# Performance work log

Hardware: AMD Instinct MI355X
Metric: run time of the kernel (lower is better)

Reference implementation:

```python
import jax, jax.numpy as jnp
import numpy as np

EMBED_DIM = 512
N_HEADS = 8
D_K = EMBED_DIM // N_HEADS

def _xavier(key, shape):
    fan_in, fan_out = shape[1], shape[0]
    limit = np.sqrt(6.0 / (fan_in + fan_out))
    return jax.random.uniform(key, shape, jnp.float32, -limit, limit)

def setup_inputs() -> dict:
    key = jax.random.key(0)
    ks = jax.random.split(key, 8)
    B, S, D = 2, 4096, EMBED_DIM
    return {
        "q": jax.random.normal(ks[0], (B, S, D), jnp.float32),
        "k": jax.random.normal(ks[1], (B, S, D), jnp.float32),
        "v": jax.random.normal(ks[2], (B, S, D), jnp.float32),
        "W_q": _xavier(ks[3], (D, D)),
        "W_k": _xavier(ks[4], (D, D)),
        "W_v": _xavier(ks[5], (D, D)),
        "W_o": _xavier(ks[6], (D, D)),
        "b_o": jnp.zeros((D,), jnp.float32),
    }

def reference(q, k, v, W_q, W_k, W_v, W_o, b_o):
    B, Sq, D = q.shape
    Sk = k.shape[1]
    # linear projections (torch Linear: x @ W.T)
    qh = (q @ W_q.T).reshape(B, Sq, N_HEADS, D_K).transpose(0, 2, 1, 3)
    kh = (k @ W_k.T).reshape(B, Sk, N_HEADS, D_K).transpose(0, 2, 1, 3)
    vh = (v @ W_v.T).reshape(B, Sk, N_HEADS, D_K).transpose(0, 2, 1, 3)
    scores = jnp.einsum('bhqd,bhkd->bhqk', qh, kh)  # [B,H,Sq,Sk]
    causal = jnp.triu(jnp.ones((Sq, Sk), bool), k=1)
    scores = jnp.where(causal, -jnp.inf, scores)
    attn = jax.nn.softmax(scores / np.sqrt(D_K), axis=-1)
    ctx = jnp.einsum('bhqk,bhkd->bhqd', attn, vh)
    ctx = ctx.transpose(0, 2, 1, 3).reshape(B, Sq, D)
    return ctx @ W_o.T + b_o
```

## Files before the change

kernel.cpp:

```cpp
#include <hip/hip_runtime.h>

typedef _Float16 f16;
typedef _Float16 f16x8 __attribute__((ext_vector_type(8)));
typedef _Float16 f16x4 __attribute__((ext_vector_type(4)));
typedef float f32x4 __attribute__((ext_vector_type(4)));
typedef float f32x16 __attribute__((ext_vector_type(16)));

#define S_TOK 4096
#define NB 2
#define NH 8
#define DKH 64
#define DMODEL 512

static __device__ __forceinline__ f32x4 mfma16(f16x8 a, f16x8 b, f32x4 c) {
    return __builtin_amdgcn_mfma_f32_16x16x32_f16(a, b, c, 0, 0, 0);
}
static __device__ __forceinline__ f32x16 mfma32(f16x8 a, f16x8 b, f32x16 c) {
    return __builtin_amdgcn_mfma_f32_32x32x16_f16(a, b, c, 0, 0, 0);
}

__global__ __launch_bounds__(256)
void proj_fused_kernel(const float* __restrict__ qx, const float* __restrict__ kx,
                       const float* __restrict__ vx,
                       const float* __restrict__ Wqp, const float* __restrict__ Wkp,
                       const float* __restrict__ Wvp,
                       f16* __restrict__ qo, f16* __restrict__ ko, f16* __restrict__ vo)
{
    const int mode = blockIdx.z;
    const float* x = (mode == 0) ? qx : (mode == 1) ? kx : vx;
    const float* W = (mode == 0) ? Wqp : (mode == 1) ? Wkp : Wvp;
    f16* out = (mode == 0) ? qo : (mode == 1) ? ko : vo;

    __shared__ f16 As[128 * 40];
    __shared__ f16 Bs[128 * 40];
    const int m0 = blockIdx.x * 128;
    const int n0 = blockIdx.y * 128;
    const int tid = threadIdx.x;
    const int wv = tid >> 6;
    const int lane = tid & 63;
    const int lr = lane & 15, lg = lane >> 4;
    const int wm = (wv >> 1) * 64, wn = (wv & 1) * 64;

    f32x4 acc[4][4];
#pragma unroll
    for (int i = 0; i < 4; ++i)
#pragma unroll
        for (int j = 0; j < 4; ++j) acc[i][j] = f32x4{0.f, 0.f, 0.f, 0.f};

    for (int kb = 0; kb < DMODEL; kb += 32) {
#pragma unroll
        for (int c = 0; c < 2; ++c) {
            const int chunk = tid + c * 256;
            const int row = chunk >> 2;
            const int col = (chunk & 3) * 8;
            const float* ga = x + (size_t)(m0 + row) * DMODEL + kb + col;
            float4 a0 = *(const float4*)ga;
            float4 a1 = *(const float4*)(ga + 4);
            f16x8 ha = { (f16)a0.x, (f16)a0.y, (f16)a0.z, (f16)a0.w,
                         (f16)a1.x, (f16)a1.y, (f16)a1.z, (f16)a1.w };
            *(f16x8*)(As + row * 40 + col) = ha;
            const float* gb = W + (size_t)(n0 + row) * DMODEL + kb + col;
            float4 b0 = *(const float4*)gb;
            float4 b1 = *(const float4*)(gb + 4);
            f16x8 hb = { (f16)b0.x, (f16)b0.y, (f16)b0.z, (f16)b0.w,
                         (f16)b1.x, (f16)b1.y, (f16)b1.z, (f16)b1.w };
            *(f16x8*)(Bs + row * 40 + col) = hb;
        }
        __syncthreads();
        f16x8 af[4], bf[4];
#pragma unroll
        for (int i = 0; i < 4; ++i)
            af[i] = *(const f16x8*)(As + (wm + 16 * i + lr) * 40 + 8 * lg);
#pragma unroll
        for (int j = 0; j < 4; ++j)
            bf[j] = *(const f16x8*)(Bs + (wn + 16 * j + lr) * 40 + 8 * lg);
#pragma unroll
        for (int i = 0; i < 4; ++i)
#pragma unroll
            for (int j = 0; j < 4; ++j)
                acc[i][j] = mfma16(af[i], bf[j], acc[i][j]);
        __syncthreads();
    }

#pragma unroll
    for (int i = 0; i < 4; ++i) {
        const int mbase = m0 + wm + 16 * i + 4 * lg;
#pragma unroll
        for (int j = 0; j < 4; ++j) {
            const int n = n0 + wn + 16 * j + lr;
            const int h = n >> 6, dk = n & 63;
            if (mode == 2) {
                const int b = mbase >> 12;
                const int s = mbase & 4095;
                f16x4 v4;
#pragma unroll
                for (int r = 0; r < 4; ++r) v4[r] = (f16)acc[i][j][r];
                *(f16x4*)(out + ((size_t)(b * NH + h) * DKH + dk) * S_TOK + s) = v4;
            } else {
                const float sc = (mode == 0) ? 0.1803368801111244f : 1.0f;
#pragma unroll
                for (int r = 0; r < 4; ++r) {
                    const int m = mbase + r;
                    const int b = m >> 12, s = m & 4095;
                    out[((size_t)(b * NH + h) * S_TOK + s) * DKH + dk] = (f16)(acc[i][j][r] * sc);
                }
            }
        }
    }
}

__global__ __launch_bounds__(256, 3)
void attn_kernel(const f16* __restrict__ qh, const f16* __restrict__ kh,
                 const f16* __restrict__ vt, f16* __restrict__ pO, float* __restrict__ pL)
{
    __shared__ f16 Ks[2][64 * 64];
    __shared__ f16 Vs[2][64 * 64];
    __shared__ f16 Ps[4][32 * 72];

    const int bid = blockIdx.x;
    const int bh = 2 * (bid & 7) + ((bid >> 3) & 1);
    const int j = bid >> 4;
    const int tid = threadIdx.x, wv = tid >> 6, lane = tid & 63;
    const int l31 = lane & 31, h = lane >> 5;

    const f16* Qp = qh + (size_t)bh * S_TOK * DKH;
    const f16* Kp = kh + (size_t)bh * S_TOK * DKH;
    const f16* Vp = vt + (size_t)bh * DKH * S_TOK;

    const int srow = tid >> 2;
    const int s0 = (tid & 3) + 4 * ((tid >> 2) & 1);
    const int s1 = s0 ^ 4;
    const int g0 = s0 ^ (srow & 7), g1 = s1 ^ (srow & 7);
    const int ldA = srow * 64 + s0 * 8, ldB = srow * 64 + s1 * 8;
    f16* Pw = &Ps[wv][0];

    for (int seg = 0; seg < 2; ++seg) {
        const int qt = seg ? (31 - j) : j;
        const int t0 = seg ? (qt + 1) : 0;
        const int t1 = seg ? (2 * qt + 2) : (j + 1);
        const int q0 = qt * 128;
        const int qw = q0 + 32 * wv + l31;
        const int unit = (bh * 32 + qt) * 2 + seg;

        f16x8 aq[4];
#pragma unroll
        for (int s = 0; s < 4; ++s)
            aq[s] = *(const f16x8*)(Qp + (size_t)qw * DKH + 16 * s + 8 * h);

        f32x16 accO0 = {}, accO1 = {};
        float mrow = -1e20f, lrow = 0.f;

        f16x8 ka = *(const f16x8*)(Kp + (size_t)(64 * t0 + srow) * DKH + g0 * 8);
        f16x8 kb = *(const f16x8*)(Kp + (size_t)(64 * t0 + srow) * DKH + g1 * 8);
        f16x8 va = *(const f16x8*)(Vp + (size_t)srow * S_TOK + 64 * t0 + g0 * 8);
        f16x8 vb = *(const f16x8*)(Vp + (size_t)srow * S_TOK + 64 * t0 + g1 * 8);
        __syncthreads();
        *(f16x8*)(&Ks[0][ldA]) = ka;  *(f16x8*)(&Ks[0][ldB]) = kb;
        *(f16x8*)(&Vs[0][ldA]) = va;  *(f16x8*)(&Vs[0][ldB]) = vb;

        int cur = 0;
        for (int t = t0; t < t1; ++t) {
            const bool pre = (t + 1 < t1);
            f16x8 kna, knb, vna, vnb;
            if (pre) {
                kna = *(const f16x8*)(Kp + (size_t)(64 * (t + 1) + srow) * DKH + g0 * 8);
                knb = *(const f16x8*)(Kp + (size_t)(64 * (t + 1) + srow) * DKH + g1 * 8);
                vna = *(const f16x8*)(Vp + (size_t)srow * S_TOK + 64 * (t + 1) + g0 * 8);
                vnb = *(const f16x8*)(Vp + (size_t)srow * S_TOK + 64 * (t + 1) + g1 * 8);
            }
            __syncthreads();
            const f16* Kb = &Ks[cur][0];
            const f16* Vb = &Vs[cur][0];

            f32x16 accS0 = {}, accS1 = {};
            __builtin_amdgcn_s_setprio(1);
#pragma unroll
            for (int s = 0; s < 4; ++s) {
                f16x8 ak0 = *(const f16x8*)(Kb + (l31) * 64 + ((2 * s + h) ^ (l31 & 7)) * 8);
                f16x8 ak1 = *(const f16x8*)(Kb + (32 + l31) * 64 + ((2 * s + h) ^ (l31 & 7)) * 8);
                accS0 = mfma32(ak0, aq[s], accS0);
                accS1 = mfma32(ak1, aq[s], accS1);
            }
            __builtin_amdgcn_s_setprio(0);

            if (t >= 2 * qt) {
#pragma unroll
                for (int e = 0; e < 16; ++e) {
                    const int kvb = 64 * t + (e & 3) + 8 * (e >> 2) + 4 * h;
                    accS0[e] = (kvb > qw) ? -1e30f : accS0[e];
                    accS1[e] = (kvb + 32 > qw) ? -1e30f : accS1[e];
                }
            }

            float tm = -1e30f;
#pragma unroll
            for (int e = 0; e < 16; ++e) tm = fmaxf(tm, fmaxf(accS0[e], accS1[e]));
            tm = fmaxf(tm, __shfl_xor(tm, 32));
            if (!__all(tm <= mrow + 8.f)) {
                const float mn = fmaxf(mrow, tm);
                const float sf = exp2f(mrow - mn);
                lrow *= sf;
                accO0 *= sf;  accO1 *= sf;
                mrow = mn;
            }
            float ts = 0.f;
#pragma unroll
            for (int g = 0; g < 4; ++g) {
                f16x4 u, u2;
#pragma unroll
                for (int r = 0; r < 4; ++r) {
                    const float p = exp2f(accS0[4 * g + r] - mrow);
                    ts += p;
                    u[r] = (f16)p;
                    const float pq = exp2f(accS1[4 * g + r] - mrow);
                    ts += pq;
                    u2[r] = (f16)pq;
                }
                *(f16x4*)(Pw + l31 * 72 + 8 * g + 4 * h) = u;
                *(f16x4*)(Pw + l31 * 72 + 32 + 8 * g + 4 * h) = u2;
            }
            ts += __shfl_xor(ts, 32);
            lrow += ts;

            __builtin_amdgcn_s_setprio(1);
#pragma unroll
            for (int s = 0; s < 4; ++s) {
                f16x8 bp = *(const f16x8*)(Pw + l31 * 72 + 16 * s + 8 * h);
                f16x8 av0 = *(const f16x8*)(Vb + (l31) * 64 + ((2 * s + h) ^ (l31 & 7)) * 8);
                f16x8 av1 = *(const f16x8*)(Vb + (32 + l31) * 64 + ((2 * s + h) ^ (l31 & 7)) * 8);
                accO0 = mfma32(av0, bp, accO0);
                accO1 = mfma32(av1, bp, accO1);
            }
            __builtin_amdgcn_s_setprio(0);

            if (pre) {
                *(f16x8*)(&Ks[cur ^ 1][ldA]) = kna;  *(f16x8*)(&Ks[cur ^ 1][ldB]) = knb;
                *(f16x8*)(&Vs[cur ^ 1][ldA]) = vna;  *(f16x8*)(&Vs[cur ^ 1][ldB]) = vnb;
            }
            cur ^= 1;
        }

        const float invl = (lrow > 0.f) ? (1.f / lrow) : 0.f;
        f16* Ob = pO + ((size_t)unit * 128 + (32 * wv + l31)) * DKH;
#pragma unroll
        for (int g = 0; g < 4; ++g) {
            f16x4 o0, o1;
#pragma unroll
            for (int r = 0; r < 4; ++r) {
                o0[r] = (f16)(accO0[4 * g + r] * invl);
                o1[r] = (f16)(accO1[4 * g + r] * invl);
            }
            *(f16x4*)(Ob + 8 * g + 4 * h) = o0;
            *(f16x4*)(Ob + 32 + 8 * g + 4 * h) = o1;
        }
        if (h == 0)
            pL[unit * 128 + 32 * wv + l31] =
                (lrow > 0.f) ? (mrow + __log2f(lrow)) : -1e30f;
    }
}

__global__ __launch_bounds__(256)
void merge_kernel(const f16* __restrict__ pO, const float* __restrict__ pL,
                  f16* __restrict__ ctx)
{
    const int tid = threadIdx.x;
    const int R = blockIdx.x * 32 + (tid >> 3);
    const int dkg = tid & 7;
    const int bh = R >> 12, q = R & 4095;
    const int qt = q >> 7, qi = q & 127;
    const int u0 = (bh * 32 + qt) * 2, u1 = u0 + 1;

    const float L0 = pL[u0 * 128 + qi];
    const float L1 = pL[u1 * 128 + qi];
    const float Lm = fmaxf(L0, L1);
    const float w0 = exp2f(L0 - Lm);
    const float w1 = exp2f(L1 - Lm);
    const float inv = 1.f / (w0 + w1);

    f16x8 a = *(const f16x8*)(pO + ((size_t)u0 * 128 + qi) * DKH + dkg * 8);
    f16x8 b = *(const f16x8*)(pO + ((size_t)u1 * 128 + qi) * DKH + dkg * 8);
    f16x8 o;
#pragma unroll
    for (int i = 0; i < 8; ++i)
        o[i] = (f16)((w0 * (float)a[i] + w1 * (float)b[i]) * inv);

    const int bb = bh >> 3, hh = bh & 7;
    *(f16x8*)(ctx + ((size_t)(bb * S_TOK + q)) * DMODEL + hh * DKH + dkg * 8) = o;
}

__global__ __launch_bounds__(256)
void oproj_kernel(const f16* __restrict__ A, const float* __restrict__ W,
                  const float* __restrict__ bias, float* __restrict__ out)
{
    __shared__ f16 As[128 * 40];
    __shared__ f16 Bs[128 * 40];
    const int m0 = blockIdx.x * 128;
    const int n0 = blockIdx.y * 128;
    const int tid = threadIdx.x;
    const int wv = tid >> 6;
    const int lane = tid & 63;
    const int lr = lane & 15, lg = lane >> 4;
    const int wm = (wv >> 1) * 64, wn = (wv & 1) * 64;

    f32x4 acc[4][4];
#pragma unroll
    for (int i = 0; i < 4; ++i)
#pragma unroll
        for (int j = 0; j < 4; ++j) acc[i][j] = f32x4{0.f, 0.f, 0.f, 0.f};

    for (int kb = 0; kb < DMODEL; kb += 32) {
#pragma unroll
        for (int c = 0; c < 2; ++c) {
            const int chunk = tid + c * 256;
            const int row = chunk >> 2;
            const int col = (chunk & 3) * 8;
            *(f16x8*)(As + row * 40 + col) =
                *(const f16x8*)(A + (size_t)(m0 + row) * DMODEL + kb + col);
            const float* gb = W + (size_t)(n0 + row) * DMODEL + kb + col;
            float4 b0 = *(const float4*)gb;
            float4 b1 = *(const float4*)(gb + 4);
            f16x8 hb = { (f16)b0.x, (f16)b0.y, (f16)b0.z, (f16)b0.w,
                         (f16)b1.x, (f16)b1.y, (f16)b1.z, (f16)b1.w };
            *(f16x8*)(Bs + row * 40 + col) = hb;
        }
        __syncthreads();
        f16x8 af[4], bf[4];
#pragma unroll
        for (int i = 0; i < 4; ++i)
            af[i] = *(const f16x8*)(As + (wm + 16 * i + lr) * 40 + 8 * lg);
#pragma unroll
        for (int j = 0; j < 4; ++j)
            bf[j] = *(const f16x8*)(Bs + (wn + 16 * j + lr) * 40 + 8 * lg);
#pragma unroll
        for (int i = 0; i < 4; ++i)
#pragma unroll
            for (int j = 0; j < 4; ++j)
                acc[i][j] = mfma16(af[i], bf[j], acc[i][j]);
        __syncthreads();
    }

#pragma unroll
    for (int i = 0; i < 4; ++i) {
        const int mbase = m0 + wm + 16 * i + 4 * lg;
#pragma unroll
        for (int j = 0; j < 4; ++j) {
            const int n = n0 + wn + 16 * j + lr;
            const float bn = bias[n];
#pragma unroll
            for (int r = 0; r < 4; ++r) {
                const int m = mbase + r;
                out[(size_t)m * DMODEL + n] = acc[i][j][r] + bn;
            }
        }
    }
}

extern "C" void kernel_launch(void* const* d_in, const int* in_sizes, int n_in,
                              void* d_out, int out_size, void* d_ws, size_t ws_size,
                              hipStream_t stream) {
    const float* q  = (const float*)d_in[0];
    const float* k  = (const float*)d_in[1];
    const float* v  = (const float*)d_in[2];
    const float* Wq = (const float*)d_in[3];
    const float* Wk = (const float*)d_in[4];
    const float* Wv = (const float*)d_in[5];
    const float* Wo = (const float*)d_in[6];
    const float* bo = (const float*)d_in[7];
    float* out = (float*)d_out;

    const size_t per = (size_t)NB * NH * S_TOK * DKH;
    f16* qh  = (f16*)d_ws;
    f16* kh  = qh + per;
    f16* vt  = kh + per;
    f16* ctx = vt + per;
    f16* pO  = ctx + per;
    float* pL = (float*)(pO + (size_t)1024 * 128 * 64);

    proj_fused_kernel<<<dim3(64, 4, 3), 256, 0, stream>>>(q, k, v, Wq, Wk, Wv, qh, kh, vt);
    attn_kernel<<<dim3(512), 256, 0, stream>>>(qh, kh, vt, pO, pL);
    merge_kernel<<<dim3(2048), 256, 0, stream>>>(pO, pL, ctx);
    oproj_kernel<<<dim3(64, 4), 256, 0, stream>>>(ctx, Wo, bo, out);
}
```

Measured before the change: 132.7 us.

## Split attention KV range into four chunks, use async LDS loads and permlane P

Each query tile's causal KV range is now split into four chunks rather than two, doubling the attention grid to 1024 blocks, and the merge kernel combines four partial results using log-sum-exp weights. K/V tiles are loaded straight into LDS with global_load_lds, replacing register staging. The P matrix is passed to the PV MFMA through permlane32_swap instead of an LDS round trip, so the Ps buffer goes away. The occupancy hint rises to 4 blocks. This trades more partial-output traffic and merge work for better load balance and less LDS traffic.

```diff
diff --git a/kernel.cpp b/kernel.cpp
--- a/kernel.cpp
+++ b/kernel.cpp
@@ -3,8 +3,10 @@
 typedef _Float16 f16;
 typedef _Float16 f16x8 __attribute__((ext_vector_type(8)));
 typedef _Float16 f16x4 __attribute__((ext_vector_type(4)));
+typedef _Float16 f16x2 __attribute__((ext_vector_type(2)));
 typedef float f32x4 __attribute__((ext_vector_type(4)));
 typedef float f32x16 __attribute__((ext_vector_type(16)));
+typedef unsigned int u32x2 __attribute__((ext_vector_type(2)));
 
 #define S_TOK 4096
 #define NB 2
@@ -17,6 +19,11 @@
 }
 static __device__ __forceinline__ f32x16 mfma32(f16x8 a, f16x8 b, f32x16 c) {
     return __builtin_amdgcn_mfma_f32_32x32x16_f16(a, b, c, 0, 0, 0);
+}
+static __device__ __forceinline__ void gl16(const f16* g, f16* l) {
+    __builtin_amdgcn_global_load_lds(
+        (const __attribute__((address_space(1))) unsigned int*)g,
+        (__attribute__((address_space(3))) unsigned int*)l, 16, 0, 0);
 }
 
 __global__ __launch_bounds__(256)
@@ -109,17 +116,17 @@
     }
 }
 
-__global__ __launch_bounds__(256, 3)
+__global__ __launch_bounds__(256, 4)
 void attn_kernel(const f16* __restrict__ qh, const f16* __restrict__ kh,
                  const f16* __restrict__ vt, f16* __restrict__ pO, float* __restrict__ pL)
 {
     __shared__ f16 Ks[2][64 * 64];
     __shared__ f16 Vs[2][64 * 64];
-    __shared__ f16 Ps[4][32 * 72];
 
     const int bid = blockIdx.x;
     const int bh = 2 * (bid & 7) + ((bid >> 3) & 1);
-    const int j = bid >> 4;
+    const int j = (bid >> 4) & 31;
+    const int cb = (bid >> 9) & 1;
     const int tid = threadIdx.x, wv = tid >> 6, lane = tid & 63;
     const int l31 = lane & 31, h = lane >> 5;
 
@@ -127,20 +134,19 @@
     const f16* Kp = kh + (size_t)bh * S_TOK * DKH;
     const f16* Vp = vt + (size_t)bh * DKH * S_TOK;
 
-    const int srow = tid >> 2;
-    const int s0 = (tid & 3) + 4 * ((tid >> 2) & 1);
-    const int s1 = s0 ^ 4;
-    const int g0 = s0 ^ (srow & 7), g1 = s1 ^ (srow & 7);
-    const int ldA = srow * 64 + s0 * 8, ldB = srow * 64 + s1 * 8;
-    f16* Pw = &Ps[wv][0];
-
+    const int srow = tid >> 3;
+    const int sg = tid & 7;
+    const int sgx = sg ^ (srow & 7);
+
+    int cur = 0;
     for (int seg = 0; seg < 2; ++seg) {
         const int qt = seg ? (31 - j) : j;
-        const int t0 = seg ? (qt + 1) : 0;
-        const int t1 = seg ? (2 * qt + 2) : (j + 1);
-        const int q0 = qt * 128;
-        const int qw = q0 + 32 * wv + l31;
-        const int unit = (bh * 32 + qt) * 2 + seg;
+        const int cc = seg ? (3 - cb) : cb;
+        const int T = 2 * qt + 2;
+        const int tb = (cc * T) >> 2;
+        const int te = ((cc + 1) * T) >> 2;
+        const int qw = qt * 128 + 32 * wv + l31;
+        const int unit = (bh * 32 + qt) * 4 + cc;
 
         f16x8 aq[4];
 #pragma unroll
@@ -150,94 +156,122 @@
         f32x16 accO0 = {}, accO1 = {};
         float mrow = -1e20f, lrow = 0.f;
 
-        f16x8 ka = *(const f16x8*)(Kp + (size_t)(64 * t0 + srow) * DKH + g0 * 8);
-        f16x8 kb = *(const f16x8*)(Kp + (size_t)(64 * t0 + srow) * DKH + g1 * 8);
-        f16x8 va = *(const f16x8*)(Vp + (size_t)srow * S_TOK + 64 * t0 + g0 * 8);
-        f16x8 vb = *(const f16x8*)(Vp + (size_t)srow * S_TOK + 64 * t0 + g1 * 8);
-        __syncthreads();
-        *(f16x8*)(&Ks[0][ldA]) = ka;  *(f16x8*)(&Ks[0][ldB]) = kb;
-        *(f16x8*)(&Vs[0][ldA]) = va;  *(f16x8*)(&Vs[0][ldB]) = vb;
-
-        int cur = 0;
-        for (int t = t0; t < t1; ++t) {
-            const bool pre = (t + 1 < t1);
-            f16x8 kna, knb, vna, vnb;
-            if (pre) {
-                kna = *(const f16x8*)(Kp + (size_t)(64 * (t + 1) + srow) * DKH + g0 * 8);
-                knb = *(const f16x8*)(Kp + (size_t)(64 * (t + 1) + srow) * DKH + g1 * 8);
-                vna = *(const f16x8*)(Vp + (size_t)srow * S_TOK + 64 * (t + 1) + g0 * 8);
-                vnb = *(const f16x8*)(Vp + (size_t)srow * S_TOK + 64 * (t + 1) + g1 * 8);
+        if (te > tb) {
+            {
+                const f16* kp1 = Kp + (size_t)(64 * tb + srow) * DKH + sgx * 8;
+                gl16(kp1, &Ks[cur][wv * 512]);
+                gl16(kp1 + 32 * DKH, &Ks[cur][2048 + wv * 512]);
+                const f16* vp1 = Vp + (size_t)srow * S_TOK + 64 * tb + sgx * 8;
+                gl16(vp1, &Vs[cur][wv * 512]);
+                gl16(vp1 + (size_t)32 * S_TOK, &Vs[cur][2048 + wv * 512]);
             }
-            __syncthreads();
-            const f16* Kb = &Ks[cur][0];
-            const f16* Vb = &Vs[cur][0];
-
-            f32x16 accS0 = {}, accS1 = {};
-            __builtin_amdgcn_s_setprio(1);
-#pragma unroll
-            for (int s = 0; s < 4; ++s) {
-                f16x8 ak0 = *(const f16x8*)(Kb + (l31) * 64 + ((2 * s + h) ^ (l31 & 7)) * 8);
-                f16x8 ak1 = *(const f16x8*)(Kb + (32 + l31) * 64 + ((2 * s + h) ^ (l31 & 7)) * 8);
-                accS0 = mfma32(ak0, aq[s], accS0);
-                accS1 = mfma32(ak1, aq[s], accS1);
+            for (int t = tb; t < te; ++t) {
+                __syncthreads();
+                if (t + 1 < te) {
+                    const f16* kp1 = Kp + (size_t)(64 * (t + 1) + srow) * DKH + sgx * 8;
+                    gl16(kp1, &Ks[cur ^ 1][wv * 512]);
+                    gl16(kp1 + 32 * DKH, &Ks[cur ^ 1][2048 + wv * 512]);
+                    const f16* vp1 = Vp + (size_t)srow * S_TOK + 64 * (t + 1) + sgx * 8;
+                    gl16(vp1, &Vs[cur ^ 1][wv * 512]);
+                    gl16(vp1 + (size_t)32 * S_TOK, &Vs[cur ^ 1][2048 + wv * 512]);
+                }
+                const f16* Kb = &Ks[cur][0];
+                const f16* Vb = &Vs[cur][0];
+
+                f32x16 accS0 = {}, accS1 = {};
+                __builtin_amdgcn_s_setprio(1);
+#pragma unroll
+                for (int s = 0; s < 4; ++s) {
+                    f16x8 ak0 = *(const f16x8*)(Kb + l31 * 64 + ((2 * s + h) ^ (l31 & 7)) * 8);
+                    f16x8 ak1 = *(const f16x8*)(Kb + (32 + l31) * 64 + ((2 * s + h) ^ (l31 & 7)) * 8);
+                    accS0 = mfma32(ak0, aq[s], accS0);
+                    accS1 = mfma32(ak1, aq[s], accS1);
+                }
+                __builtin_amdgcn_s_setprio(0);
+
+                if (t >= 2 * qt) {
+#pragma unroll
+                    for (int e = 0; e < 16; ++e) {
+                        const int kvb = 64 * t + (e & 3) + 8 * (e >> 2) + 4 * h;
+                        accS0[e] = (kvb > qw) ? -1e30f : accS0[e];
+                        accS1[e] = (kvb + 32 > qw) ? -1e30f : accS1[e];
+                    }
+                }
+
+                float tm = -1e30f;
+#pragma unroll
+                for (int e = 0; e < 16; ++e) tm = fmaxf(tm, fmaxf(accS0[e], accS1[e]));
+                tm = fmaxf(tm, __shfl_xor(tm, 32));
+                if (!__all(tm <= mrow + 8.f)) {
+                    const float mn = fmaxf(mrow, tm);
+                    const float sf = exp2f(mrow - mn);
+                    lrow *= sf;
+                    accO0 *= sf;  accO1 *= sf;
+                    mrow = mn;
+                }
+
+                float ts = 0.f;
+                {
+                    unsigned int Xd0[4], Xd1[4];
+#pragma unroll
+                    for (int g = 0; g < 4; ++g) {
+                        float p0 = exp2f(accS0[4 * g + 0] - mrow);
+                        float p1 = exp2f(accS0[4 * g + 1] - mrow);
+                        float p2 = exp2f(accS0[4 * g + 2] - mrow);
+                        float p3 = exp2f(accS0[4 * g + 3] - mrow);
+                        ts += (p0 + p1) + (p2 + p3);
+                        union { f16x2 hh; unsigned int u; } a0, a1;
+                        a0.hh = f16x2{(f16)p0, (f16)p1};
+                        a1.hh = f16x2{(f16)p2, (f16)p3};
+                        Xd0[g] = a0.u;  Xd1[g] = a1.u;
+                    }
+                    __builtin_amdgcn_s_setprio(1);
+#pragma unroll
+                    for (int sp = 0; sp < 2; ++sp) {
+                        u32x2 rA = __builtin_amdgcn_permlane32_swap(Xd0[2 * sp], Xd0[2 * sp + 1], false, false);
+                        u32x2 rB = __builtin_amdgcn_permlane32_swap(Xd1[2 * sp], Xd1[2 * sp + 1], false, false);
+                        union { unsigned int u[4]; f16x8 v; } F;
+                        F.u[0] = rA[0]; F.u[1] = rB[0]; F.u[2] = rA[1]; F.u[3] = rB[1];
+                        f16x8 av0 = *(const f16x8*)(Vb + l31 * 64 + ((2 * sp + h) ^ (l31 & 7)) * 8);
+                        f16x8 av1 = *(const f16x8*)(Vb + (32 + l31) * 64 + ((2 * sp + h) ^ (l31 & 7)) * 8);
+                        accO0 = mfma32(av0, F.v, accO0);
+                        accO1 = mfma32(av1, F.v, accO1);
+                    }
+                    __builtin_amdgcn_s_setprio(0);
+                }
+                {
+                    unsigned int Xd0[4], Xd1[4];
+#pragma unroll
+                    for (int g = 0; g < 4; ++g) {
+                        float p0 = exp2f(accS1[4 * g + 0] - mrow);
+                        float p1 = exp2f(accS1[4 * g + 1] - mrow);
+                        float p2 = exp2f(accS1[4 * g + 2] - mrow);
+                        float p3 = exp2f(accS1[4 * g + 3] - mrow);
+                        ts += (p0 + p1) + (p2 + p3);
+                        union { f16x2 hh; unsigned int u; } a0, a1;
+                        a0.hh = f16x2{(f16)p0, (f16)p1};
+                        a1.hh = f16x2{(f16)p2, (f16)p3};
+                        Xd0[g] = a0.u;  Xd1[g] = a1.u;
+                    }
+                    __builtin_amdgcn_s_setprio(1);
+#pragma unroll
+                    for (int sp = 0; sp < 2; ++sp) {
+                        const int spp = 2 + sp;
+                        u32x2 rA = __builtin_amdgcn_permlane32_swap(Xd0[2 * sp], Xd0[2 * sp + 1], false, false);
+                        u32x2 rB = __builtin_amdgcn_permlane32_swap(Xd1[2 * sp], Xd1[2 * sp + 1], false, false);
+                        union { unsigned int u[4]; f16x8 v; } F;
+                        F.u[0] = rA[0]; F.u[1] = rB[0]; F.u[2] = rA[1]; F.u[3] = rB[1];
+                        f16x8 av0 = *(const f16x8*)(Vb + l31 * 64 + ((2 * spp + h) ^ (l31 & 7)) * 8);
+                        f16x8 av1 = *(const f16x8*)(Vb + (32 + l31) * 64 + ((2 * spp + h) ^ (l31 & 7)) * 8);
+                        accO0 = mfma32(av0, F.v, accO0);
+                        accO1 = mfma32(av1, F.v, accO1);
+                    }
+                    __builtin_amdgcn_s_setprio(0);
+                }
+                ts += __shfl_xor(ts, 32);
+                lrow += ts;
+                cur ^= 1;
             }
-            __builtin_amdgcn_s_setprio(0);
-
-            if (t >= 2 * qt) {
-#pragma unroll
-                for (int e = 0; e < 16; ++e) {
-                    const int kvb = 64 * t + (e & 3) + 8 * (e >> 2) + 4 * h;
-                    accS0[e] = (kvb > qw) ? -1e30f : accS0[e];
-                    accS1[e] = (kvb + 32 > qw) ? -1e30f : accS1[e];
-                }
-            }
-
-            float tm = -1e30f;
-#pragma unroll
-            for (int e = 0; e < 16; ++e) tm = fmaxf(tm, fmaxf(accS0[e], accS1[e]));
-            tm = fmaxf(tm, __shfl_xor(tm, 32));
-            if (!__all(tm <= mrow + 8.f)) {
-                const float mn = fmaxf(mrow, tm);
-                const float sf = exp2f(mrow - mn);
-                lrow *= sf;
-                accO0 *= sf;  accO1 *= sf;
-                mrow = mn;
-            }
-            float ts = 0.f;
-#pragma unroll
-            for (int g = 0; g < 4; ++g) {
-                f16x4 u, u2;
-#pragma unroll
-                for (int r = 0; r < 4; ++r) {
-                    const float p = exp2f(accS0[4 * g + r] - mrow);
-                    ts += p;
-                    u[r] = (f16)p;
-                    const float pq = exp2f(accS1[4 * g + r] - mrow);
-                    ts += pq;
-                    u2[r] = (f16)pq;
-                }
-                *(f16x4*)(Pw + l31 * 72 + 8 * g + 4 * h) = u;
-                *(f16x4*)(Pw + l31 * 72 + 32 + 8 * g + 4 * h) = u2;
-            }
-            ts += __shfl_xor(ts, 32);
-            lrow += ts;
-
-            __builtin_amdgcn_s_setprio(1);
-#pragma unroll
-            for (int s = 0; s < 4; ++s) {
-                f16x8 bp = *(const f16x8*)(Pw + l31 * 72 + 16 * s + 8 * h);
-                f16x8 av0 = *(const f16x8*)(Vb + (l31) * 64 + ((2 * s + h) ^ (l31 & 7)) * 8);
-                f16x8 av1 = *(const f16x8*)(Vb + (32 + l31) * 64 + ((2 * s + h) ^ (l31 & 7)) * 8);
-                accO0 = mfma32(av0, bp, accO0);
-                accO1 = mfma32(av1, bp, accO1);
-            }
-            __builtin_amdgcn_s_setprio(0);
-
-            if (pre) {
-                *(f16x8*)(&Ks[cur ^ 1][ldA]) = kna;  *(f16x8*)(&Ks[cur ^ 1][ldB]) = knb;
-                *(f16x8*)(&Vs[cur ^ 1][ldA]) = vna;  *(f16x8*)(&Vs[cur ^ 1][ldB]) = vnb;
-            }
-            cur ^= 1;
         }
 
         const float invl = (lrow > 0.f) ? (1.f / lrow) : 0.f;
@@ -268,24 +302,32 @@
     const int dkg = tid & 7;
     const int bh = R >> 12, q = R & 4095;
     const int qt = q >> 7, qi = q & 127;
-    const int u0 = (bh * 32 + qt) * 2, u1 = u0 + 1;
-
-    const float L0 = pL[u0 * 128 + qi];
-    const float L1 = pL[u1 * 128 + qi];
-    const float Lm = fmaxf(L0, L1);
-    const float w0 = exp2f(L0 - Lm);
-    const float w1 = exp2f(L1 - Lm);
-    const float inv = 1.f / (w0 + w1);
-
-    f16x8 a = *(const f16x8*)(pO + ((size_t)u0 * 128 + qi) * DKH + dkg * 8);
-    f16x8 b = *(const f16x8*)(pO + ((size_t)u1 * 128 + qi) * DKH + dkg * 8);
-    f16x8 o;
-#pragma unroll
-    for (int i = 0; i < 8; ++i)
-        o[i] = (f16)((w0 * (float)a[i] + w1 * (float)b[i]) * inv);
+    const int ub = (bh * 32 + qt) * 4;
+
+    float L[4];
+#pragma unroll
+    for (int c = 0; c < 4; ++c) L[c] = pL[(ub + c) * 128 + qi];
+    float Lm = fmaxf(fmaxf(L[0], L[1]), fmaxf(L[2], L[3]));
+    float w[4], wsum = 0.f;
+#pragma unroll
+    for (int c = 0; c < 4; ++c) { w[c] = exp2f(L[c] - Lm); wsum += w[c]; }
+    const float inv = 1.f / wsum;
+
+    float o[8];
+#pragma unroll
+    for (int i = 0; i < 8; ++i) o[i] = 0.f;
+#pragma unroll
+    for (int c = 0; c < 4; ++c) {
+        f16x8 a = *(const f16x8*)(pO + ((size_t)(ub + c) * 128 + qi) * DKH + dkg * 8);
+#pragma unroll
+        for (int i = 0; i < 8; ++i) o[i] += w[c] * (float)a[i];
+    }
+    f16x8 ov;
+#pragma unroll
+    for (int i = 0; i < 8; ++i) ov[i] = (f16)(o[i] * inv);
 
     const int bb = bh >> 3, hh = bh & 7;
-    *(f16x8*)(ctx + ((size_t)(bb * S_TOK + q)) * DMODEL + hh * DKH + dkg * 8) = o;
+    *(f16x8*)(ctx + ((size_t)(bb * S_TOK + q)) * DMODEL + hh * DKH + dkg * 8) = ov;
 }
 
 __global__ __launch_bounds__(256)
@@ -374,10 +416,10 @@
     f16* vt  = kh + per;
     f16* ctx = vt + per;
     f16* pO  = ctx + per;
-    float* pL = (float*)(pO + (size_t)1024 * 128 * 64);
+    float* pL = (float*)(pO + (size_t)2048 * 128 * 64);
 
     proj_fused_kernel<<<dim3(64, 4, 3), 256, 0, stream>>>(q, k, v, Wq, Wk, Wv, qh, kh, vt);
-    attn_kernel<<<dim3(512), 256, 0, stream>>>(qh, kh, vt, pO, pL);
+    attn_kernel<<<dim3(1024), 256, 0, stream>>>(qh, kh, vt, pO, pL);
     merge_kernel<<<dim3(2048), 256, 0, stream>>>(pO, pL, ctx);
     oproj_kernel<<<dim3(64, 4), 256, 0, stream>>>(ctx, Wo, bo, out);
 }
```

After: 136.5 us. 1.03x slower.
